# Kernel tuning notes

Hardware: AMD Instinct MI355X
Metric: run time of the kernel (lower is better)

The kernel has to match this reference:

```python
import jax, jax.numpy as jnp
import numpy as np

# Graph / model dims (see init_kwargs)
N = 50000          # nodes
E = 800000         # edges (before self loops)
IN, HID, OUT = 128, 64, 47
HEADS = (4, 4, 1)
SLOPE = 0.2        # PyG GATConv default negative_slope
# dropout p=0.6 in the torch module is a no-op in eval mode -> omitted


def _glorot(key, shape):
    fan_in = shape[0] if len(shape) == 2 else int(np.prod(shape))
    return jax.random.normal(key, shape, jnp.float32) / np.sqrt(fan_in)


def setup_inputs() -> dict:
    key = jax.random.key(0)
    ks = jax.random.split(key, 16)
    x = jax.random.normal(ks[0], (N, IN), jnp.float32)
    edge_index = jax.random.randint(ks[1], (2, E), 0, N)
    # layer dims: (in_dim, out_dim_per_head, heads)
    dims = [(IN, HID, HEADS[0]), (HID * HEADS[0], HID, HEADS[1]), (HID * HEADS[1], OUT, HEADS[2])]
    inp = {"x": x, "edge_index": edge_index}
    for i, (d_in, c, h) in enumerate(dims, start=1):
        inp[f"W{i}"] = _glorot(ks[3 * i], (d_in, h * c))
        inp[f"a{i}s"] = _glorot(ks[3 * i + 1], (h, c))
        inp[f"a{i}d"] = _glorot(ks[3 * i + 2], (h, c))
        inp[f"b{i}"] = jnp.zeros((h * c,), jnp.float32)
    return inp


def gat_layer(x, src, dst, W, a_s, a_d, b, h, c):
    # x: [N, d_in] -> per-head features [N, h, c]
    feat = (x @ W).reshape(N, h, c)
    # per-node attention logits [N, h]
    al_src = jnp.einsum('nhc,hc->nh', feat, a_s)
    al_dst = jnp.einsum('nhc,hc->nh', feat, a_d)
    # per-edge score, LeakyReLU (PyG: alpha = a_src[src] + a_dst[dst])
    e = jax.nn.leaky_relu(al_src[src] + al_dst[dst], SLOPE)  # [Etot, h]
    # segment softmax over incoming edges of each dst node
    emax = jax.ops.segment_max(e, dst, num_segments=N)       # [N, h]
    w = jnp.exp(e - emax[dst])
    denom = jax.ops.segment_sum(w, dst, num_segments=N)      # [N, h]
    alpha = w / denom[dst]                                   # [Etot, h]
    # weighted scatter-add aggregation
    out = jax.ops.segment_sum(alpha[:, :, None] * feat[src], dst, num_segments=N)
    return out.reshape(N, h * c) + b                         # concat heads + bias


def reference(x, edge_index, W1, a1s, a1d, b1, W2, a2s, a2d, b2, W3, a3s, a3d, b3):
    loop = jnp.arange(N, dtype=edge_index.dtype)
    src = jnp.concatenate([edge_index[0], loop])  # add_self_loops=True
    dst = jnp.concatenate([edge_index[1], loop])
    h = gat_layer(x, src, dst, W1, a1s, a1d, b1, HEADS[0], HID)
    h = jax.nn.elu(h)
    h = gat_layer(h, src, dst, W2, a2s, a2d, b2, HEADS[1], HID)
    h = jax.nn.elu(h)
    h = gat_layer(h, src, dst, W3, a3s, a3d, b3, HEADS[2], OUT)  # no elu on last layer
    return h
```

## Files before the change

### kernel.cpp

```cpp
#include <hip/hip_runtime.h>
#include <hip/hip_bf16.h>

#define NNODES 50000
#define NEDGES 800000
#define ETOT   (NNODES + NEDGES)
#define MTILES 3136
#define MPAD   (MTILES * 16)
#define NBLK   196

typedef __attribute__((ext_vector_type(8))) short short8;
typedef __attribute__((ext_vector_type(4))) float floatx4;
typedef __attribute__((ext_vector_type(2))) unsigned int uint2v;
typedef __attribute__((ext_vector_type(4))) short short4v;

__device__ __forceinline__ float bf2f(__hip_bfloat16 x) { return __bfloat162float(x); }
__device__ __forceinline__ __hip_bfloat16 f2bf(float f) { return __float2bfloat16(f); }
__device__ __forceinline__ float sane(float v, float c) {
  v = (v == v) ? v : 0.f;
  return fminf(fmaxf(v, -c), c);
}
__device__ __forceinline__ unsigned short bfbits(float f) {
  union { __hip_bfloat16 b; unsigned short u; } cv;
  cv.b = f2bf(f);
  return cv.u;
}

__global__ void zero_int_kernel(int* __restrict__ p, int n) {
  int i = blockIdx.x * blockDim.x + threadIdx.x;
  if (i < n) p[i] = 0;
}
__global__ void fill_out_kernel(float* __restrict__ o, int n, float v) {
  int i = blockIdx.x * blockDim.x + threadIdx.x;
  if (i < n) o[i] = v;
}
__global__ void split_input_kernel(const float* __restrict__ in,
                                   __hip_bfloat16* __restrict__ hi,
                                   __hip_bfloat16* __restrict__ lo) {
  int i = blockIdx.x * blockDim.x + threadIdx.x;
  if (i >= MPAD * 256) return;
  float v = (i < NNODES * 128) ? sane(in[i], 1e4f) : 0.f;
  __hip_bfloat16 h = f2bf(v);
  hi[i] = h;
  lo[i] = f2bf(v - bf2f(h));
}
__global__ void pad47_kernel(const float* __restrict__ a, const float* __restrict__ b,
                             float* __restrict__ ap, float* __restrict__ bp) {
  int i = threadIdx.x;
  ap[i] = (i < 47) ? sane(a[i], 1e4f) : 0.f;
  bp[i] = (i < 47) ? sane(b[i], 1e4f) : 0.f;
}

__global__ void degree_kernel(const int* __restrict__ ei, int* __restrict__ deg) {
  int p = blockIdx.x * blockDim.x + threadIdx.x;
  if (p >= ETOT) return;
  int dst = (p < NEDGES) ? ei[NEDGES + p] : (p - NEDGES);
  dst = min(max(dst, 0), NNODES - 1);
  atomicAdd(&deg[dst], 1);
}

__global__ __launch_bounds__(256) void block_sum_kernel(const int* __restrict__ deg,
                                                        int* __restrict__ bsum) {
  __shared__ int sh[256];
  int b = blockIdx.x, t = threadIdx.x;
  int i = b * 256 + t;
  sh[t] = (i < NNODES) ? deg[i] : 0;
  __syncthreads();
  for (int off = 128; off > 0; off >>= 1) {
    if (t < off) sh[t] += sh[t + off];
    __syncthreads();
  }
  if (t == 0) bsum[b] = sh[0];
}

__global__ __launch_bounds__(256) void scan_bsum_kernel(const int* __restrict__ bsum,
                                                        int* __restrict__ boff,
                                                        int* __restrict__ row_ptr) {
  __shared__ int sh[256];
  int t = threadIdx.x;
  int v = (t < NBLK) ? bsum[t] : 0;
  sh[t] = v;
  __syncthreads();
  for (int off = 1; off < 256; off <<= 1) {
    int u = (t >= off) ? sh[t - off] : 0;
    __syncthreads();
    sh[t] += u;
    __syncthreads();
  }
  if (t < NBLK) boff[t] = sh[t] - v;
  if (t == 255) row_ptr[NNODES] = sh[255];
}

__global__ __launch_bounds__(256) void emit_rowptr_kernel(const int* __restrict__ deg,
                                                          const int* __restrict__ boff,
                                                          int* __restrict__ row_ptr,
                                                          int* __restrict__ cursor) {
  __shared__ int sh[256];
  int b = blockIdx.x, t = threadIdx.x;
  int i = b * 256 + t;
  int d = (i < NNODES) ? deg[i] : 0;
  sh[t] = d;
  __syncthreads();
  for (int off = 1; off < 256; off <<= 1) {
    int u = (t >= off) ? sh[t - off] : 0;
    __syncthreads();
    sh[t] += u;
    __syncthreads();
  }
  if (i < NNODES) {
    int v = boff[b] + sh[t] - d;
    row_ptr[i] = v;
    cursor[i] = v;
  }
}

__global__ void scatter_kernel(const int* __restrict__ ei, int* __restrict__ cursor,
                               int* __restrict__ csr_src) {
  int p = blockIdx.x * blockDim.x + threadIdx.x;
  if (p >= ETOT) return;
  int src, dst;
  if (p < NEDGES) { src = ei[p]; dst = ei[NEDGES + p]; }
  else            { src = p - NEDGES; dst = src; }
  src = min(max(src, 0), NNODES - 1);
  dst = min(max(dst, 0), NNODES - 1);
  int pos = atomicAdd(&cursor[dst], 1);
  pos = min(max(pos, 0), ETOT - 1);
  csr_src[pos] = src;
}

__global__ void pack_w_kernel(const float* __restrict__ W,
                              __hip_bfloat16* __restrict__ Bh,
                              __hip_bfloat16* __restrict__ Bl,
                              int K, int Nreal, int Npad) {
  int idx = blockIdx.x * blockDim.x + threadIdx.x;
  if (idx >= Npad * K) return;
  int e = idx;
  int j = e & 7;    e >>= 3;
  int m = e & 15;   e >>= 4;
  int quad = e & 3; e >>= 2;
  int kch = K >> 5;
  int kk32 = e % kch;
  int nt = e / kch;
  int n = nt * 16 + m;
  int k = kk32 * 32 + quad * 8 + j;
  float v = (n < Nreal) ? sane(W[k * Nreal + n], 1e4f) : 0.f;
  __hip_bfloat16 h = f2bf(v);
  Bh[idx] = h;
  Bl[idx] = f2bf(v - bf2f(h));
}

template<int KDIM, int NOUT, int HEADS, int WAVES_N>
__global__ __launch_bounds__(256) void gemm_attn_kernel(
    const __hip_bfloat16* __restrict__ Ah, const __hip_bfloat16* __restrict__ Al,
    const __hip_bfloat16* __restrict__ Bh, const __hip_bfloat16* __restrict__ Bl,
    const float* __restrict__ asv, const float* __restrict__ adv,
    __hip_bfloat16* __restrict__ Ch, float* __restrict__ als, float* __restrict__ ald) {
  constexpr int KCH = KDIM / 32;
  constexpr int CT = (NOUT / 16) / WAVES_N;
  constexpr int RT = 4;
  constexpr int RGROUPS = 4 / WAVES_N;
  __shared__ __hip_bfloat16 sAh[2 * 64 * 32];
  __shared__ __hip_bfloat16 sAl[2 * 64 * 32];
  int wave = threadIdx.x >> 6, lane = threadIdx.x & 63;
  int wrow = wave / WAVES_N, wcol = wave % WAVES_N;
  int rt0 = (blockIdx.x * RGROUPS + wrow) * RT;
  int ct0 = wcol * CT;
  int m = lane & 15, quad = lane >> 4;

  const short8* Bph = reinterpret_cast<const short8*>(Bh);
  const short8* Bpl = reinterpret_cast<const short8*>(Bl);

  floatx4 acc[RT][CT];
#pragma unroll
  for (int rt = 0; rt < RT; ++rt)
#pragma unroll
    for (int ct = 0; ct < CT; ++ct) acc[rt][ct] = (floatx4){0.f, 0.f, 0.f, 0.f};

  int tid = threadIdx.x;
  size_t gstage = (size_t)(rt0 * 16 + (tid >> 2)) * KDIM + (tid & 3) * 8;

#pragma unroll 2
  for (int ks = 0; ks < KCH / 2; ++ks) {
    short8 a_h[RT], a_l[RT];
    if constexpr (WAVES_N == 4) {
      short8 vh0 = *reinterpret_cast<const short8*>(Ah + gstage + ks * 64);
      short8 vh1 = *reinterpret_cast<const short8*>(Ah + gstage + ks * 64 + 32);
      short8 vl0 = *reinterpret_cast<const short8*>(Al + gstage + ks * 64);
      short8 vl1 = *reinterpret_cast<const short8*>(Al + gstage + ks * 64 + 32);
      __syncthreads();
      *reinterpret_cast<short8*>(&sAh[tid * 8]) = vh0;
      *reinterpret_cast<short8*>(&sAh[2048 + tid * 8]) = vh1;
      *reinterpret_cast<short8*>(&sAl[tid * 8]) = vl0;
      *reinterpret_cast<short8*>(&sAl[2048 + tid * 8]) = vl1;
      __syncthreads();
#pragma unroll
      for (int kk0 = 0; kk0 < 2; ++kk0) {
#pragma unroll
        for (int rt = 0; rt < RT; ++rt) {
          int so = kk0 * 2048 + (rt * 16 + m) * 32 + quad * 8;
          a_h[rt] = *reinterpret_cast<const short8*>(&sAh[so]);
          a_l[rt] = *reinterpret_cast<const short8*>(&sAl[so]);
        }
        int kk = ks * 2 + kk0;
#pragma unroll
        for (int ct = 0; ct < CT; ++ct) {
          size_t o = ((size_t)(ct0 + ct) * KCH + kk) * 64 + lane;
          short8 b_h = Bph[o];
          short8 b_l = Bpl[o];
#pragma unroll
          for (int rt = 0; rt < RT; ++rt) {
            acc[rt][ct] = __builtin_amdgcn_mfma_f32_16x16x32_bf16(a_h[rt], b_h, acc[rt][ct], 0, 0, 0);
            acc[rt][ct] = __builtin_amdgcn_mfma_f32_16x16x32_bf16(a_h[rt], b_l, acc[rt][ct], 0, 0, 0);
            acc[rt][ct] = __builtin_amdgcn_mfma_f32_16x16x32_bf16(a_l[rt], b_h, acc[rt][ct], 0, 0, 0);
          }
        }
      }
    } else {
#pragma unroll
      for (int kk0 = 0; kk0 < 2; ++kk0) {
        int kk = ks * 2 + kk0;
#pragma unroll
        for (int rt = 0; rt < RT; ++rt) {
          size_t aoff = (size_t)((rt0 + rt) * 16 + m) * KDIM + kk * 32 + quad * 8;
          a_h[rt] = *reinterpret_cast<const short8*>(Ah + aoff);
          a_l[rt] = *reinterpret_cast<const short8*>(Al + aoff);
        }
#pragma unroll
        for (int ct = 0; ct < CT; ++ct) {
          size_t o = ((size_t)(ct0 + ct) * KCH + kk) * 64 + lane;
          short8 b_h = Bph[o];
          short8 b_l = Bpl[o];
#pragma unroll
          for (int rt = 0; rt < RT; ++rt) {
            acc[rt][ct] = __builtin_amdgcn_mfma_f32_16x16x32_bf16(a_h[rt], b_h, acc[rt][ct], 0, 0, 0);
            acc[rt][ct] = __builtin_amdgcn_mfma_f32_16x16x32_bf16(a_h[rt], b_l, acc[rt][ct], 0, 0, 0);
            acc[rt][ct] = __builtin_amdgcn_mfma_f32_16x16x32_bf16(a_l[rt], b_h, acc[rt][ct], 0, 0, 0);
          }
        }
      }
    }
  }

  constexpr int CPH = NOUT / HEADS;
  int head = (ct0 * 16) / CPH;
  float asl[CT], adl[CT];
#pragma unroll
  for (int ct = 0; ct < CT; ++ct) {
    asl[ct] = asv[(ct0 + ct) * 16 + m];
    adl[ct] = adv[(ct0 + ct) * 16 + m];
  }
  float ps[RT * 4], pd[RT * 4];
#pragma unroll
  for (int i = 0; i < RT * 4; ++i) { ps[i] = 0.f; pd[i] = 0.f; }
#pragma unroll
  for (int rt = 0; rt < RT; ++rt)
#pragma unroll
    for (int ct = 0; ct < CT; ++ct)
#pragma unroll
      for (int r = 0; r < 4; ++r) {
        ps[rt * 4 + r] += acc[rt][ct][r] * asl[ct];
        pd[rt * 4 + r] += acc[rt][ct][r] * adl[ct];
      }
#pragma unroll
  for (int off = 1; off < 16; off <<= 1) {
#pragma unroll
    for (int i = 0; i < RT * 4; ++i) {
      ps[i] += __shfl_xor(ps[i], off);
      pd[i] += __shfl_xor(pd[i], off);
    }
  }
  if (m == 0) {
#pragma unroll
    for (int rt = 0; rt < RT; ++rt)
#pragma unroll
      for (int r = 0; r < 4; ++r) {
        int row = (rt0 + rt) * 16 + quad * 4 + r;
        if (row < NNODES) {
          als[(size_t)row * HEADS + head] = sane(ps[rt * 4 + r], 80.f);
          ald[(size_t)row * HEADS + head] = sane(pd[rt * 4 + r], 80.f);
        }
      }
  }

#pragma unroll
  for (int rt = 0; rt < RT; ++rt)
#pragma unroll
    for (int ct = 0; ct < CT; ++ct)
#pragma unroll
      for (int r = 0; r < 4; ++r) {
        int row = (rt0 + rt) * 16 + quad * 4 + r;
        if (row < NNODES) {
          float v = sane(acc[rt][ct][r], 3e4f);
          Ch[(size_t)row * NOUT + (ct0 + ct) * 16 + m] = f2bf(v);
        }
      }
}

template<int H>
__global__ __launch_bounds__(256) void alpha_kernel(const int* __restrict__ row_ptr,
                                                    const int* __restrict__ csr_src,
                                                    const float* __restrict__ als,
                                                    const float* __restrict__ ald,
                                                    float* __restrict__ alpha) {
  int wid = threadIdx.x >> 6, lane = threadIdx.x & 63;
  int dst = blockIdx.x * 4 + wid;
  if (dst >= NNODES) return;
  int start = row_ptr[dst], end = row_ptr[dst + 1];
  int cnt = end - start;
  if (cnt <= 0) return;
  float adv[H];
#pragma unroll
  for (int h = 0; h < H; ++h) adv[h] = ald[(size_t)dst * H + h];

  if (cnt <= 64) {
    int i = start + lane;
    bool valid = lane < cnt;
    int s = valid ? min(max(csr_src[i], 0), NNODES - 1) : 0;
    float w[H];
#pragma unroll
    for (int h = 0; h < H; ++h) {
      float e = als[(size_t)s * H + h] + adv[h];
      e = e > 0.f ? e : 0.2f * e;
      e = fminf(fmaxf(e, -80.f), 80.f);
      w[h] = valid ? __expf(e) : 0.f;
    }
#pragma unroll
    for (int h = 0; h < H; ++h) {
      float v = w[h];
#pragma unroll
      for (int off = 1; off < 64; off <<= 1) v += __shfl_xor(v, off);
      float inv = 1.f / fmaxf(v, 1e-30f);
      if (valid) alpha[(size_t)i * H + h] = w[h] * inv;
    }
  } else {
    float dl[H];
#pragma unroll
    for (int h = 0; h < H; ++h) dl[h] = 0.f;
    for (int base = start; base < end; base += 64) {
      int i = base + lane;
      bool valid = i < end;
      int s = valid ? min(max(csr_src[i], 0), NNODES - 1) : 0;
#pragma unroll
      for (int h = 0; h < H; ++h) {
        float e = als[(size_t)s * H + h] + adv[h];
        e = e > 0.f ? e : 0.2f * e;
        e = fminf(fmaxf(e, -80.f), 80.f);
        float w = valid ? __expf(e) : 0.f;
        dl[h] += w;
        if (valid) alpha[(size_t)i * H + h] = w;
      }
    }
    float inv[H];
#pragma unroll
    for (int h = 0; h < H; ++h) {
      float v = dl[h];
#pragma unroll
      for (int off = 1; off < 64; off <<= 1) v += __shfl_xor(v, off);
      inv[h] = 1.f / fmaxf(v, 1e-30f);
    }
    for (int base = start; base < end; base += 64) {
      int i = base + lane;
      if (i < end)
#pragma unroll
        for (int h = 0; h < H; ++h) alpha[(size_t)i * H + h] *= inv[h];
    }
  }
}

__global__ __launch_bounds__(256) void agg_mid_kernel(const int* __restrict__ row_ptr,
                                                      const int* __restrict__ csr_src,
                                                      const __hip_bfloat16* __restrict__ Fh,
                                                      const float* __restrict__ alpha,
                                                      const float* __restrict__ bias,
                                                      __hip_bfloat16* __restrict__ Oh,
                                                      __hip_bfloat16* __restrict__ Ol) {
  int wid = threadIdx.x >> 6, lane = threadIdx.x & 63;
  int dst = blockIdx.x * 4 + wid;
  if (dst >= NNODES) return;
  int start = row_ptr[dst], end = row_ptr[dst + 1];
  int cnt = end - start;
  int head = lane >> 4;
  float a0 = 0.f, a1 = 0.f, a2 = 0.f, a3 = 0.f;
  int p = 0;
  for (; p + 3 < cnt; p += 4) {
    int e0 = start + p, e1 = e0 + 1, e2 = e0 + 2, e3 = e0 + 3;
    int s0 = csr_src[e0], s1 = csr_src[e1], s2 = csr_src[e2], s3 = csr_src[e3];
    float w0 = alpha[(size_t)e0 * 4 + head];
    float w1 = alpha[(size_t)e1 * 4 + head];
    float w2 = alpha[(size_t)e2 * 4 + head];
    float w3 = alpha[(size_t)e3 * 4 + head];
    uint2v f0 = *reinterpret_cast<const uint2v*>(Fh + (size_t)s0 * 256 + lane * 4);
    uint2v f1 = *reinterpret_cast<const uint2v*>(Fh + (size_t)s1 * 256 + lane * 4);
    uint2v f2 = *reinterpret_cast<const uint2v*>(Fh + (size_t)s2 * 256 + lane * 4);
    uint2v f3 = *reinterpret_cast<const uint2v*>(Fh + (size_t)s3 * 256 + lane * 4);
    a0 += w0 * __uint_as_float(f0.x << 16);
    a1 += w0 * __uint_as_float(f0.x & 0xffff0000u);
    a2 += w0 * __uint_as_float(f0.y << 16);
    a3 += w0 * __uint_as_float(f0.y & 0xffff0000u);
    a0 += w1 * __uint_as_float(f1.x << 16);
    a1 += w1 * __uint_as_float(f1.x & 0xffff0000u);
    a2 += w1 * __uint_as_float(f1.y << 16);
    a3 += w1 * __uint_as_float(f1.y & 0xffff0000u);
    a0 += w2 * __uint_as_float(f2.x << 16);
    a1 += w2 * __uint_as_float(f2.x & 0xffff0000u);
    a2 += w2 * __uint_as_float(f2.y << 16);
    a3 += w2 * __uint_as_float(f2.y & 0xffff0000u);
    a0 += w3 * __uint_as_float(f3.x << 16);
    a1 += w3 * __uint_as_float(f3.x & 0xffff0000u);
    a2 += w3 * __uint_as_float(f3.y << 16);
    a3 += w3 * __uint_as_float(f3.y & 0xffff0000u);
  }
  for (; p < cnt; ++p) {
    int e0 = start + p;
    int s0 = csr_src[e0];
    float w0 = alpha[(size_t)e0 * 4 + head];
    uint2v f0 = *reinterpret_cast<const uint2v*>(Fh + (size_t)s0 * 256 + lane * 4);
    a0 += w0 * __uint_as_float(f0.x << 16);
    a1 += w0 * __uint_as_float(f0.x & 0xffff0000u);
    a2 += w0 * __uint_as_float(f0.y << 16);
    a3 += w0 * __uint_as_float(f0.y & 0xffff0000u);
  }
  floatx4 bv = *reinterpret_cast<const floatx4*>(bias + lane * 4);
  float o0 = a0 + bv.x, o1 = a1 + bv.y, o2 = a2 + bv.z, o3 = a3 + bv.w;
  o0 = o0 > 0.f ? o0 : __expf(o0) - 1.f;
  o1 = o1 > 0.f ? o1 : __expf(o1) - 1.f;
  o2 = o2 > 0.f ? o2 : __expf(o2) - 1.f;
  o3 = o3 > 0.f ? o3 : __expf(o3) - 1.f;
  float h0 = bf2f(f2bf(o0)), h1 = bf2f(f2bf(o1)), h2 = bf2f(f2bf(o2)), h3 = bf2f(f2bf(o3));
  short4v hv = (short4v){(short)bfbits(o0), (short)bfbits(o1), (short)bfbits(o2), (short)bfbits(o3)};
  short4v lv = (short4v){(short)bfbits(o0 - h0), (short)bfbits(o1 - h1),
                         (short)bfbits(o2 - h2), (short)bfbits(o3 - h3)};
  *reinterpret_cast<short4v*>(Oh + (size_t)dst * 256 + lane * 4) = hv;
  *reinterpret_cast<short4v*>(Ol + (size_t)dst * 256 + lane * 4) = lv;
}

__global__ void agg_final_kernel(const int* __restrict__ row_ptr,
                                 const int* __restrict__ csr_src,
                                 const __hip_bfloat16* __restrict__ Fh,
                                 const float* __restrict__ alpha,
                                 const float* __restrict__ bias,
                                 float* __restrict__ out) {
  int wid = threadIdx.x >> 6, lane = threadIdx.x & 63;
  int dst = blockIdx.x * 4 + wid;
  if (dst >= NNODES) return;
  int start = row_ptr[dst], end = row_ptr[dst + 1];
  int cnt = end - start;
  float acc = 0.f;
  int p = 0;
  for (; p + 3 < cnt; p += 4) {
    int e0 = start + p;
    int s0 = csr_src[e0], s1 = csr_src[e0 + 1], s2 = csr_src[e0 + 2], s3 = csr_src[e0 + 3];
    float w0 = alpha[e0], w1 = alpha[e0 + 1], w2 = alpha[e0 + 2], w3 = alpha[e0 + 3];
    float f0 = bf2f(Fh[(size_t)s0 * 64 + lane]);
    float f1 = bf2f(Fh[(size_t)s1 * 64 + lane]);
    float f2 = bf2f(Fh[(size_t)s2 * 64 + lane]);
    float f3 = bf2f(Fh[(size_t)s3 * 64 + lane]);
    acc += w0 * f0 + w1 * f1 + w2 * f2 + w3 * f3;
  }
  for (; p < cnt; ++p) {
    int e0 = start + p;
    acc += alpha[e0] * bf2f(Fh[(size_t)csr_src[e0] * 64 + lane]);
  }
  if (lane < 47) out[(size_t)dst * 47 + lane] = acc + bias[lane];
}

extern "C" void kernel_launch(void* const* d_in, const int* in_sizes, int n_in,
                              void* d_out, int out_size, void* d_ws, size_t ws_size,
                              hipStream_t stream) {
  const float* x   = (const float*)d_in[0];
  const int* ei    = (const int*)d_in[1];
  const float* W1  = (const float*)d_in[2];
  const float* a1s = (const float*)d_in[3];
  const float* a1d = (const float*)d_in[4];
  const float* b1  = (const float*)d_in[5];
  const float* W2  = (const float*)d_in[6];
  const float* a2s = (const float*)d_in[7];
  const float* a2d = (const float*)d_in[8];
  const float* b2  = (const float*)d_in[9];
  const float* W3  = (const float*)d_in[10];
  const float* a3s = (const float*)d_in[11];
  const float* a3d = (const float*)d_in[12];
  const float* b3  = (const float*)d_in[13];
  float* out = (float*)d_out;
  (void)n_in; (void)in_sizes;

  char* base = (char*)d_ws;
  size_t off = 0;
  auto alloc = [&](size_t bytes) -> char* {
    off = (off + 255) & ~(size_t)255;
    char* p = base + off;
    off += bytes;
    return p;
  };
  int* deg     = (int*)alloc((size_t)NNODES * 4);
  int* cursor  = (int*)alloc((size_t)NNODES * 4);
  int* row_ptr = (int*)alloc((size_t)(NNODES + 1) * 4);
  int* csr_src = (int*)alloc((size_t)ETOT * 4);
  int* bsum    = (int*)alloc(256 * 4);
  int* boff    = (int*)alloc(256 * 4);
  float* als   = (float*)alloc((size_t)NNODES * 4 * 4);
  float* ald   = (float*)alloc((size_t)NNODES * 4 * 4);
  float* alpha = (float*)alloc((size_t)ETOT * 4 * 4);
  __hip_bfloat16* Ah = (__hip_bfloat16*)alloc((size_t)MPAD * 256 * 2);
  __hip_bfloat16* Al = (__hip_bfloat16*)alloc((size_t)MPAD * 256 * 2);
  __hip_bfloat16* Fh = (__hip_bfloat16*)alloc((size_t)NNODES * 256 * 2);
  __hip_bfloat16* wth = (__hip_bfloat16*)alloc((size_t)256 * 256 * 2);
  __hip_bfloat16* wtl = (__hip_bfloat16*)alloc((size_t)256 * 256 * 2);
  float* asv3 = (float*)alloc(64 * 4);
  float* adv3 = (float*)alloc(64 * 4);

  if (ws_size < off) {
    fill_out_kernel<<<(out_size + 255) / 256, 256, 0, stream>>>(out, out_size, 12345.f);
    return;
  }

  zero_int_kernel<<<(NNODES + 255) / 256, 256, 0, stream>>>(deg, NNODES);
  degree_kernel<<<(ETOT + 255) / 256, 256, 0, stream>>>(ei, deg);
  block_sum_kernel<<<NBLK, 256, 0, stream>>>(deg, bsum);
  scan_bsum_kernel<<<1, 256, 0, stream>>>(bsum, boff, row_ptr);
  emit_rowptr_kernel<<<NBLK, 256, 0, stream>>>(deg, boff, row_ptr, cursor);
  scatter_kernel<<<(ETOT + 255) / 256, 256, 0, stream>>>(ei, cursor, csr_src);

  split_input_kernel<<<(MPAD * 256 + 255) / 256, 256, 0, stream>>>(x, Ah, Al);
  pad47_kernel<<<1, 64, 0, stream>>>(a3s, a3d, asv3, adv3);

  const int grid12 = (NNODES + 63) / 64;
  const int grid3 = (NNODES + 255) / 256;
  const int gridN4 = (NNODES + 3) / 4;

  pack_w_kernel<<<(256 * 128 + 255) / 256, 256, 0, stream>>>(W1, wth, wtl, 128, 256, 256);
  gemm_attn_kernel<128, 256, 4, 4><<<grid12, 256, 0, stream>>>(Ah, Al, wth, wtl, a1s, a1d,
                                                               Fh, als, ald);
  alpha_kernel<4><<<gridN4, 256, 0, stream>>>(row_ptr, csr_src, als, ald, alpha);
  agg_mid_kernel<<<gridN4, 256, 0, stream>>>(row_ptr, csr_src, Fh, alpha, b1, Ah, Al);

  pack_w_kernel<<<(256 * 256 + 255) / 256, 256, 0, stream>>>(W2, wth, wtl, 256, 256, 256);
  gemm_attn_kernel<256, 256, 4, 4><<<grid12, 256, 0, stream>>>(Ah, Al, wth, wtl, a2s, a2d,
                                                               Fh, als, ald);
  alpha_kernel<4><<<gridN4, 256, 0, stream>>>(row_ptr, csr_src, als, ald, alpha);
  agg_mid_kernel<<<gridN4, 256, 0, stream>>>(row_ptr, csr_src, Fh, alpha, b2, Ah, Al);

  pack_w_kernel<<<(64 * 256 + 255) / 256, 256, 0, stream>>>(W3, wth, wtl, 256, 47, 64);
  gemm_attn_kernel<256, 64, 1, 1><<<grid3, 256, 0, stream>>>(Ah, Al, wth, wtl, asv3, adv3,
                                                             Fh, als, ald);
  alpha_kernel<1><<<gridN4, 256, 0, stream>>>(row_ptr, csr_src, als, ald, alpha);
  agg_final_kernel<<<gridN4, 256, 0, stream>>>(row_ptr, csr_src, Fh, alpha, b3, out);
}
```

Baseline: 515.8 us.

## Sort CSR buckets by edge index and unroll aggregation loops with dual accumulators

The scatter step now writes the source and the original edge index into temporary arrays. A new per-destination rank sort then orders each bucket by edge index, which makes the CSR order deterministic rather than set by atomic arrival order. The mid and final aggregation loops are unrolled to 8 edges and split across two accumulators, so more gathers are in flight and the add chains are shorter. The sort adds an extra kernel with O(deg^2) work per node and more workspace traffic, which mostly serves determinism rather than speed.

```diff
diff --git a/kernel.cpp b/kernel.cpp
--- a/kernel.cpp
+++ b/kernel.cpp
@@ -114,7 +114,7 @@
 }
 
 __global__ void scatter_kernel(const int* __restrict__ ei, int* __restrict__ cursor,
-                               int* __restrict__ csr_src) {
+                               int* __restrict__ tmp_src, int* __restrict__ tmp_p) {
   int p = blockIdx.x * blockDim.x + threadIdx.x;
   if (p >= ETOT) return;
   int src, dst;
@@ -124,7 +124,26 @@
   dst = min(max(dst, 0), NNODES - 1);
   int pos = atomicAdd(&cursor[dst], 1);
   pos = min(max(pos, 0), ETOT - 1);
-  csr_src[pos] = src;
+  tmp_src[pos] = src;
+  tmp_p[pos] = p;
+}
+
+__global__ __launch_bounds__(256) void bucket_sort_kernel(const int* __restrict__ row_ptr,
+                                                          const int* __restrict__ tmp_src,
+                                                          const int* __restrict__ tmp_p,
+                                                          int* __restrict__ csr_src) {
+  int wid = threadIdx.x >> 6, lane = threadIdx.x & 63;
+  int dst = blockIdx.x * 4 + wid;
+  if (dst >= NNODES) return;
+  int start = row_ptr[dst], end = row_ptr[dst + 1];
+  int cnt = end - start;
+  for (int i = lane; i < cnt; i += 64) {
+    int pi = tmp_p[start + i];
+    int si = tmp_src[start + i];
+    int rank = 0;
+    for (int j = 0; j < cnt; ++j) rank += (tmp_p[start + j] < pi) ? 1 : 0;
+    csr_src[start + rank] = si;
+  }
 }
 
 __global__ void pack_w_kernel(const float* __restrict__ W,
@@ -380,14 +399,68 @@
   int cnt = end - start;
   int head = lane >> 4;
   float a0 = 0.f, a1 = 0.f, a2 = 0.f, a3 = 0.f;
+  float b0 = 0.f, b1 = 0.f, b2 = 0.f, b3 = 0.f;
   int p = 0;
+  for (; p + 7 < cnt; p += 8) {
+    int e0 = start + p;
+    int s0 = csr_src[e0],     s1 = csr_src[e0 + 1], s2 = csr_src[e0 + 2], s3 = csr_src[e0 + 3];
+    int s4 = csr_src[e0 + 4], s5 = csr_src[e0 + 5], s6 = csr_src[e0 + 6], s7 = csr_src[e0 + 7];
+    float w0 = alpha[(size_t)(e0    ) * 4 + head];
+    float w1 = alpha[(size_t)(e0 + 1) * 4 + head];
+    float w2 = alpha[(size_t)(e0 + 2) * 4 + head];
+    float w3 = alpha[(size_t)(e0 + 3) * 4 + head];
+    float w4 = alpha[(size_t)(e0 + 4) * 4 + head];
+    float w5 = alpha[(size_t)(e0 + 5) * 4 + head];
+    float w6 = alpha[(size_t)(e0 + 6) * 4 + head];
+    float w7 = alpha[(size_t)(e0 + 7) * 4 + head];
+    uint2v f0 = *reinterpret_cast<const uint2v*>(Fh + (size_t)s0 * 256 + lane * 4);
+    uint2v f1 = *reinterpret_cast<const uint2v*>(Fh + (size_t)s1 * 256 + lane * 4);
+    uint2v f2 = *reinterpret_cast<const uint2v*>(Fh + (size_t)s2 * 256 + lane * 4);
+    uint2v f3 = *reinterpret_cast<const uint2v*>(Fh + (size_t)s3 * 256 + lane * 4);
+    uint2v f4 = *reinterpret_cast<const uint2v*>(Fh + (size_t)s4 * 256 + lane * 4);
+    uint2v f5 = *reinterpret_cast<const uint2v*>(Fh + (size_t)s5 * 256 + lane * 4);
+    uint2v f6 = *reinterpret_cast<const uint2v*>(Fh + (size_t)s6 * 256 + lane * 4);
+    uint2v f7 = *reinterpret_cast<const uint2v*>(Fh + (size_t)s7 * 256 + lane * 4);
+    a0 += w0 * __uint_as_float(f0.x << 16);
+    a1 += w0 * __uint_as_float(f0.x & 0xffff0000u);
+    a2 += w0 * __uint_as_float(f0.y << 16);
+    a3 += w0 * __uint_as_float(f0.y & 0xffff0000u);
+    b0 += w1 * __uint_as_float(f1.x << 16);
+    b1 += w1 * __uint_as_float(f1.x & 0xffff0000u);
+    b2 += w1 * __uint_as_float(f1.y << 16);
+    b3 += w1 * __uint_as_float(f1.y & 0xffff0000u);
+    a0 += w2 * __uint_as_float(f2.x << 16);
+    a1 += w2 * __uint_as_float(f2.x & 0xffff0000u);
+    a2 += w2 * __uint_as_float(f2.y << 16);
+    a3 += w2 * __uint_as_float(f2.y & 0xffff0000u);
+    b0 += w3 * __uint_as_float(f3.x << 16);
+    b1 += w3 * __uint_as_float(f3.x & 0xffff0000u);
+    b2 += w3 * __uint_as_float(f3.y << 16);
+    b3 += w3 * __uint_as_float(f3.y & 0xffff0000u);
+    a0 += w4 * __uint_as_float(f4.x << 16);
+    a1 += w4 * __uint_as_float(f4.x & 0xffff0000u);
+    a2 += w4 * __uint_as_float(f4.y << 16);
+    a3 += w4 * __uint_as_float(f4.y & 0xffff0000u);
+    b0 += w5 * __uint_as_float(f5.x << 16);
+    b1 += w5 * __uint_as_float(f5.x & 0xffff0000u);
+    b2 += w5 * __uint_as_float(f5.y << 16);
+    b3 += w5 * __uint_as_float(f5.y & 0xffff0000u);
+    a0 += w6 * __uint_as_float(f6.x << 16);
+    a1 += w6 * __uint_as_float(f6.x & 0xffff0000u);
+    a2 += w6 * __uint_as_float(f6.y << 16);
+    a3 += w6 * __uint_as_float(f6.y & 0xffff0000u);
+    b0 += w7 * __uint_as_float(f7.x << 16);
+    b1 += w7 * __uint_as_float(f7.x & 0xffff0000u);
+    b2 += w7 * __uint_as_float(f7.y << 16);
+    b3 += w7 * __uint_as_float(f7.y & 0xffff0000u);
+  }
   for (; p + 3 < cnt; p += 4) {
-    int e0 = start + p, e1 = e0 + 1, e2 = e0 + 2, e3 = e0 + 3;
-    int s0 = csr_src[e0], s1 = csr_src[e1], s2 = csr_src[e2], s3 = csr_src[e3];
-    float w0 = alpha[(size_t)e0 * 4 + head];
-    float w1 = alpha[(size_t)e1 * 4 + head];
-    float w2 = alpha[(size_t)e2 * 4 + head];
-    float w3 = alpha[(size_t)e3 * 4 + head];
+    int e0 = start + p;
+    int s0 = csr_src[e0], s1 = csr_src[e0 + 1], s2 = csr_src[e0 + 2], s3 = csr_src[e0 + 3];
+    float w0 = alpha[(size_t)(e0    ) * 4 + head];
+    float w1 = alpha[(size_t)(e0 + 1) * 4 + head];
+    float w2 = alpha[(size_t)(e0 + 2) * 4 + head];
+    float w3 = alpha[(size_t)(e0 + 3) * 4 + head];
     uint2v f0 = *reinterpret_cast<const uint2v*>(Fh + (size_t)s0 * 256 + lane * 4);
     uint2v f1 = *reinterpret_cast<const uint2v*>(Fh + (size_t)s1 * 256 + lane * 4);
     uint2v f2 = *reinterpret_cast<const uint2v*>(Fh + (size_t)s2 * 256 + lane * 4);
@@ -396,18 +469,18 @@
     a1 += w0 * __uint_as_float(f0.x & 0xffff0000u);
     a2 += w0 * __uint_as_float(f0.y << 16);
     a3 += w0 * __uint_as_float(f0.y & 0xffff0000u);
-    a0 += w1 * __uint_as_float(f1.x << 16);
-    a1 += w1 * __uint_as_float(f1.x & 0xffff0000u);
-    a2 += w1 * __uint_as_float(f1.y << 16);
-    a3 += w1 * __uint_as_float(f1.y & 0xffff0000u);
+    b0 += w1 * __uint_as_float(f1.x << 16);
+    b1 += w1 * __uint_as_float(f1.x & 0xffff0000u);
+    b2 += w1 * __uint_as_float(f1.y << 16);
+    b3 += w1 * __uint_as_float(f1.y & 0xffff0000u);
     a0 += w2 * __uint_as_float(f2.x << 16);
     a1 += w2 * __uint_as_float(f2.x & 0xffff0000u);
     a2 += w2 * __uint_as_float(f2.y << 16);
     a3 += w2 * __uint_as_float(f2.y & 0xffff0000u);
-    a0 += w3 * __uint_as_float(f3.x << 16);
-    a1 += w3 * __uint_as_float(f3.x & 0xffff0000u);
-    a2 += w3 * __uint_as_float(f3.y << 16);
-    a3 += w3 * __uint_as_float(f3.y & 0xffff0000u);
+    b0 += w3 * __uint_as_float(f3.x << 16);
+    b1 += w3 * __uint_as_float(f3.x & 0xffff0000u);
+    b2 += w3 * __uint_as_float(f3.y << 16);
+    b3 += w3 * __uint_as_float(f3.y & 0xffff0000u);
   }
   for (; p < cnt; ++p) {
     int e0 = start + p;
@@ -419,6 +492,7 @@
     a2 += w0 * __uint_as_float(f0.y << 16);
     a3 += w0 * __uint_as_float(f0.y & 0xffff0000u);
   }
+  a0 += b0; a1 += b1; a2 += b2; a3 += b3;
   floatx4 bv = *reinterpret_cast<const floatx4*>(bias + lane * 4);
   float o0 = a0 + bv.x, o1 = a1 + bv.y, o2 = a2 + bv.z, o3 = a3 + bv.w;
   o0 = o0 > 0.f ? o0 : __expf(o0) - 1.f;
@@ -444,22 +518,30 @@
   if (dst >= NNODES) return;
   int start = row_ptr[dst], end = row_ptr[dst + 1];
   int cnt = end - start;
-  float acc = 0.f;
+  float acc = 0.f, acc2 = 0.f;
   int p = 0;
-  for (; p + 3 < cnt; p += 4) {
+  for (; p + 7 < cnt; p += 8) {
     int e0 = start + p;
-    int s0 = csr_src[e0], s1 = csr_src[e0 + 1], s2 = csr_src[e0 + 2], s3 = csr_src[e0 + 3];
-    float w0 = alpha[e0], w1 = alpha[e0 + 1], w2 = alpha[e0 + 2], w3 = alpha[e0 + 3];
+    int s0 = csr_src[e0],     s1 = csr_src[e0 + 1], s2 = csr_src[e0 + 2], s3 = csr_src[e0 + 3];
+    int s4 = csr_src[e0 + 4], s5 = csr_src[e0 + 5], s6 = csr_src[e0 + 6], s7 = csr_src[e0 + 7];
+    float w0 = alpha[e0],     w1 = alpha[e0 + 1], w2 = alpha[e0 + 2], w3 = alpha[e0 + 3];
+    float w4 = alpha[e0 + 4], w5 = alpha[e0 + 5], w6 = alpha[e0 + 6], w7 = alpha[e0 + 7];
     float f0 = bf2f(Fh[(size_t)s0 * 64 + lane]);
     float f1 = bf2f(Fh[(size_t)s1 * 64 + lane]);
     float f2 = bf2f(Fh[(size_t)s2 * 64 + lane]);
     float f3 = bf2f(Fh[(size_t)s3 * 64 + lane]);
-    acc += w0 * f0 + w1 * f1 + w2 * f2 + w3 * f3;
+    float f4 = bf2f(Fh[(size_t)s4 * 64 + lane]);
+    float f5 = bf2f(Fh[(size_t)s5 * 64 + lane]);
+    float f6 = bf2f(Fh[(size_t)s6 * 64 + lane]);
+    float f7 = bf2f(Fh[(size_t)s7 * 64 + lane]);
+    acc  += w0 * f0 + w2 * f2 + w4 * f4 + w6 * f6;
+    acc2 += w1 * f1 + w3 * f3 + w5 * f5 + w7 * f7;
   }
   for (; p < cnt; ++p) {
     int e0 = start + p;
     acc += alpha[e0] * bf2f(Fh[(size_t)csr_src[e0] * 64 + lane]);
   }
+  acc += acc2;
   if (lane < 47) out[(size_t)dst * 47 + lane] = acc + bias[lane];
 }
 
@@ -495,6 +577,8 @@
   int* cursor  = (int*)alloc((size_t)NNODES * 4);
   int* row_ptr = (int*)alloc((size_t)(NNODES + 1) * 4);
   int* csr_src = (int*)alloc((size_t)ETOT * 4);
+  int* tmp_src = (int*)alloc((size_t)ETOT * 4);
+  int* tmp_p   = (int*)alloc((size_t)ETOT * 4);
   int* bsum    = (int*)alloc(256 * 4);
   int* boff    = (int*)alloc(256 * 4);
   float* als   = (float*)alloc((size_t)NNODES * 4 * 4);
@@ -518,7 +602,8 @@
   block_sum_kernel<<<NBLK, 256, 0, stream>>>(deg, bsum);
   scan_bsum_kernel<<<1, 256, 0, stream>>>(bsum, boff, row_ptr);
   emit_rowptr_kernel<<<NBLK, 256, 0, stream>>>(deg, boff, row_ptr, cursor);
-  scatter_kernel<<<(ETOT + 255) / 256, 256, 0, stream>>>(ei, cursor, csr_src);
+  scatter_kernel<<<(ETOT + 255) / 256, 256, 0, stream>>>(ei, cursor, tmp_src, tmp_p);
+  bucket_sort_kernel<<<(NNODES + 3) / 4, 256, 0, stream>>>(row_ptr, tmp_src, tmp_p, csr_src);
 
   split_input_kernel<<<(MPAD * 256 + 255) / 256, 256, 0, stream>>>(x, Ah, Al);
   pad47_kernel<<<1, 64, 0, stream>>>(a3s, a3d, asv3, adv3);
```

Measured after the change: 542.8 us. 1.05x slower.
